# Optimization experiments

Measured on AMD Instinct MI355X. Metric: run time of the kernel, lower is better.

The kernel has to match this reference:

```python
import jax, jax.numpy as jnp
import numpy as np

D_MODEL = 2048
N_HEADS = 16
HEAD_DIM = D_MODEL // N_HEADS  # 128
B, S, PAST = 2, 2048, 2048


def setup_inputs() -> dict:
    key = jax.random.key(0)
    ks = jax.random.split(key, 7)
    sc = 0.02
    return {
        "x": jax.random.normal(ks[0], (B, S, D_MODEL), dtype=jnp.float32),
        "past_k": jax.random.normal(ks[1], (B, N_HEADS, PAST, HEAD_DIM), dtype=jnp.float32),
        "past_v": jax.random.normal(ks[2], (B, N_HEADS, PAST, HEAD_DIM), dtype=jnp.float32),
        "Wq": jax.random.normal(ks[3], (D_MODEL, D_MODEL), dtype=jnp.float32) * sc,
        "Wk": jax.random.normal(ks[4], (D_MODEL, D_MODEL), dtype=jnp.float32) * sc,
        "Wv": jax.random.normal(ks[5], (D_MODEL, D_MODEL), dtype=jnp.float32) * sc,
        "Wo": jax.random.normal(ks[6], (D_MODEL, D_MODEL), dtype=jnp.float32) * sc,
    }


def reference(x, past_k, past_v, Wq, Wk, Wv, Wo):
    b, s, d = x.shape
    # nn.Linear(bias=False): y = x @ W.T ; split heads -> (B, H, S, hd)
    def proj_heads(W):
        return (x @ W.T).reshape(b, s, N_HEADS, HEAD_DIM).transpose(0, 2, 1, 3)
    q = proj_heads(Wq)
    k = proj_heads(Wk)
    v = proj_heads(Wv)
    # KV-cache append along sequence axis
    k = jnp.concatenate([past_k, k], axis=2)  # (B, H, full_S, hd)
    v = jnp.concatenate([past_v, v], axis=2)
    present = (k, v)
    full_s = k.shape[2]
    scores = jnp.einsum("bhqd,bhkd->bhqk", q, k) / (HEAD_DIM ** 0.5)
    # causal mask: query i (global pos past+i) may attend keys j <= past+i
    offset = full_s - s
    qi = jnp.arange(s)[:, None]
    kj = jnp.arange(full_s)[None, :]
    mask = kj > (qi + offset)  # triu with diagonal = full_s - s + 1
    scores = jnp.where(mask[None, None], -jnp.inf, scores)
    attn = jax.nn.softmax(scores, axis=-1)
    out = jnp.einsum("bhqk,bhkd->bhqd", attn, v)
    out = out.transpose(0, 2, 1, 3).reshape(b, s, d)
    output = out @ Wo.T
    return output, present
```

## Files before the change

### kernel.cpp

```cpp
#include <hip/hip_runtime.h>
#include <hip/hip_bf16.h>
#include <stdint.h>

typedef __attribute__((ext_vector_type(8))) short bf16x8;
typedef __attribute__((ext_vector_type(4))) float f32x4;
typedef __attribute__((ext_vector_type(16))) float f32x16;
typedef unsigned short u16;
typedef unsigned int u32;
typedef const __attribute__((address_space(1))) u32* gp_t;
typedef __attribute__((address_space(3))) u32* lp_t;

#define HD 128
#define NH 16
#define SEQ 2048
#define PASTN 2048
#define FULLS 4096
#define DM 2048

__device__ __forceinline__ u16 f2b(float f){
  union { float f; u32 u; } v; v.f = f;
  return (u16)((v.u + 0x7fffu + ((v.u >> 16) & 1u)) >> 16);
}
__device__ __forceinline__ float b2f(u16 b){
  union { u32 u; float f; } v; v.u = ((u32)b) << 16;
  return v.f;
}
__device__ __forceinline__ u32 cvtpk(float lo, float hi){
  u32 r; asm("v_cvt_pk_bf16_f32 %0, %1, %2" : "=v"(r) : "v"(lo), "v"(hi)); return r;
}
__device__ __forceinline__ f32x16 zero16(){ f32x16 z = {}; return z; }

__global__ void k_conv5(const float* __restrict__ sx,
                        const float* __restrict__ s1, const float* __restrict__ s2,
                        const float* __restrict__ s3, const float* __restrict__ s4,
                        u16* __restrict__ dx,
                        u16* __restrict__ d1, u16* __restrict__ d2,
                        u16* __restrict__ d3, u16* __restrict__ d4)
{
  const int total = 2097152 + 4 * 1048576;
  int i = blockIdx.x * blockDim.x + threadIdx.x;
  int stride = gridDim.x * blockDim.x;
  for (; i < total; i += stride){
    const float* s; u16* d; int off;
    if (i < 2097152){ s = sx; d = dx; off = i; }
    else {
      int t = i - 2097152;
      int seg = t >> 20; off = t & 1048575;
      s = (seg == 0) ? s1 : (seg == 1) ? s2 : (seg == 2) ? s3 : s4;
      d = (seg == 0) ? d1 : (seg == 1) ? d2 : (seg == 2) ? d3 : d4;
    }
    float4 v = ((const float4*)s)[off];
    ushort4 o = { f2b(v.x), f2b(v.y), f2b(v.z), f2b(v.w) };
    ((ushort4*)d)[off] = o;
  }
}

__global__ __launch_bounds__(512, 1)
void k_qkv_fused(const u16* __restrict__ A,
                 const u16* __restrict__ Bq, const u16* __restrict__ Bk,
                 const u16* __restrict__ Bv,
                 u16* __restrict__ qb, u16* __restrict__ kbb,
                 u16* __restrict__ vtb,
                 float* __restrict__ outk, float* __restrict__ outv,
                 const float* __restrict__ pk, const float* __restrict__ pv)
{
  __shared__ char LDS[131072];
  const int bx = blockIdx.x;
  const int tid = threadIdx.x;

  if (bx >= 384){
    if (bx < 448){
      for (int i = (bx - 384) * 512 + tid; i < 2097152; i += 32768){
        int g = i * 4;
        int c = g & 127;
        int r = g >> 7;
        int bh = r >> 11;
        int s = r & 2047;
        long dst = ((long)bh * FULLS + s) * HD + c;
        float4 v = ((const float4*)pk)[i];
        *(float4*)(outk + dst) = v;
        ushort4 o = { f2b(v.x), f2b(v.y), f2b(v.z), f2b(v.w) };
        *(ushort4*)(kbb + dst) = o;
      }
    } else {
      float* ldsF = (float*)LDS;
      for (int cc = 0; cc < 16; cc++){
        int c = ((bx - 448) << 4) + cc;
        int bh = c >> 5, s0 = (c & 31) << 6;
        const float* src = pv + ((long)bh * PASTN + s0) * HD;
        float* dsv = outv + ((long)bh * FULLS + s0) * HD;
#pragma unroll
        for (int p = 0; p < 4; p++){
          int idx = tid + p * 512;
          int row = idx >> 5, c4 = (idx & 31) << 2;
          float4 v = *(const float4*)(src + row * HD + c4);
          *(float4*)(dsv + row * HD + c4) = v;
          ldsF[row * 129 + c4 + 0] = v.x;
          ldsF[row * 129 + c4 + 1] = v.y;
          ldsF[row * 129 + c4 + 2] = v.z;
          ldsF[row * 129 + c4 + 3] = v.w;
        }
        __syncthreads();
        int d = tid >> 2, sb = (tid & 3) << 4;
        u16* dst = vtb + ((long)bh * HD + d) * FULLS + s0 + sb;
#pragma unroll
        for (int g = 0; g < 4; g++){
          ushort4 o = { f2b(ldsF[(sb + g * 4 + 0) * 129 + d]),
                        f2b(ldsF[(sb + g * 4 + 1) * 129 + d]),
                        f2b(ldsF[(sb + g * 4 + 2) * 129 + d]),
                        f2b(ldsF[(sb + g * 4 + 3) * 129 + d]) };
          *(ushort4*)(dst + g * 4) = o;
        }
        __syncthreads();
      }
    }
    return;
  }

  const int w = tid >> 6, l = tid & 63;
  const int wm = w >> 2, wn = w & 3;
  const int which = bx >> 7;
  const int r0 = bx & 127;
  const int m0 = (r0 & 15) * 256;
  const int n0s = (r0 >> 4) * 256;
  const u16* Bm = (which == 0) ? Bq : (which == 1) ? Bk : Bv;

  const int aoff0 = (((l >> 4) * 16) ^ ((l & 7) << 4));
  const int aoff1 = ((64 + (l >> 4) * 16) ^ ((l & 7) << 4));
  const char* ArdB = LDS + wm * 16384 + (l & 15) * 128;
  const char* BrdB = LDS + 65536 + (wn >> 1) * 16384 + (wn & 1) * 8192 + (l & 15) * 128;

  const int Pa = tid * 16, Pb = tid * 16 + 8192;
  const int ra = Pa >> 7, rb = Pb >> 7;
  const int sro1 = ra * 2048 + ((((Pa & 127) ^ ((ra & 7) << 4))) >> 1);
  const int sro2 = rb * 2048 + ((((Pb & 127) ^ ((rb & 7) << 4))) >> 1);
  char* sd1 = LDS + w * 1024;
  char* sd2 = LDS + w * 1024 + 8192;

  f32x4 acc[8][4] = {};

#define GLDS(SRC, DST) __builtin_amdgcn_global_load_lds((gp_t)(const void*)(SRC), (lp_t)(void*)(DST), 16, 0, 0)
#define STG(MAT, ROWB, C, REG) { const u16* s_ = (MAT) + (long)(ROWB) * 2048 + (C) * 64; \
    GLDS(s_ + sro1, sd1 + (REG)); GLDS(s_ + sro2, sd2 + (REG)); }
#define RDB(DST, PAR) { _Pragma("unroll") for (int nf = 0; nf < 4; nf++){ \
      DST[nf*2]   = *(const bf16x8*)(BrdB + (PAR)*32768 + nf*2048 + aoff0); \
      DST[nf*2+1] = *(const bf16x8*)(BrdB + (PAR)*32768 + nf*2048 + aoff1); } }
#define RDA(PAR, MF) \
      a0 = *(const bf16x8*)(ArdB + (PAR)*32768 + (MF)*2048 + aoff0); \
      a1 = *(const bf16x8*)(ArdB + (PAR)*32768 + (MF)*2048 + aoff1); \
      a2 = *(const bf16x8*)(ArdB + (PAR)*32768 + (MF+1)*2048 + aoff0); \
      a3 = *(const bf16x8*)(ArdB + (PAR)*32768 + (MF+1)*2048 + aoff1);
#define BARW { __builtin_amdgcn_s_barrier(); \
      asm volatile("s_waitcnt lgkmcnt(0)" ::: "memory"); \
      __builtin_amdgcn_sched_barrier(0); }
#define MM(BF, MF) { __builtin_amdgcn_s_setprio(1); \
      _Pragma("unroll") for (int nf = 0; nf < 4; nf++){ \
        acc[MF][nf]   = __builtin_amdgcn_mfma_f32_16x16x32_bf16(a0, BF[nf*2],   acc[MF][nf],   0,0,0); \
        acc[MF][nf]   = __builtin_amdgcn_mfma_f32_16x16x32_bf16(a1, BF[nf*2+1], acc[MF][nf],   0,0,0); \
        acc[MF+1][nf] = __builtin_amdgcn_mfma_f32_16x16x32_bf16(a2, BF[nf*2],   acc[MF+1][nf], 0,0,0); \
        acc[MF+1][nf] = __builtin_amdgcn_mfma_f32_16x16x32_bf16(a3, BF[nf*2+1], acc[MF+1][nf], 0,0,0); } \
      __builtin_amdgcn_s_setprio(0); }

  STG(A,  m0,        0, 0);
  STG(A,  m0 + 128,  0, 16384);
  STG(Bm, n0s,       0, 65536);
  STG(Bm, n0s + 128, 0, 81920);
  STG(Bm, n0s,       1, 98304);
  STG(Bm, n0s + 128, 1, 114688);
  asm volatile("s_waitcnt vmcnt(4)" ::: "memory");
  __builtin_amdgcn_s_barrier();

  for (int i = 0; i < 16; ++i){
    const int c1 = 2 * i + 1;
    const int cn = 2 * i + 2;
    const bool nlast = (i < 15);
    bf16x8 b0[8], b1[8];
    bf16x8 a0, a1, a2, a3;

    RDB(b0, 0); RDA(0, 0);
    STG(A, m0, c1, 32768);
    BARW; MM(b0, 0);
    __builtin_amdgcn_s_barrier();

    RDA(0, 2);
    STG(A, m0 + 128, c1, 49152);
    BARW; MM(b0, 2);
    __builtin_amdgcn_s_barrier();

    RDA(0, 4);
    if (nlast) STG(Bm, n0s, cn, 65536);
    BARW; MM(b0, 4);
    __builtin_amdgcn_s_barrier();

    RDA(0, 6);
    if (nlast) STG(Bm, n0s + 128, cn, 81920);
    BARW; MM(b0, 6);
    if (nlast) { asm volatile("s_waitcnt vmcnt(4)" ::: "memory"); }
    else       { asm volatile("s_waitcnt vmcnt(0)" ::: "memory"); }
    __builtin_amdgcn_s_barrier();

    RDB(b1, 1); RDA(1, 0);
    if (nlast) STG(A, m0, cn, 0);
    BARW; MM(b1, 0);
    __builtin_amdgcn_s_barrier();

    RDA(1, 2);
    if (nlast) STG(A, m0 + 128, cn, 16384);
    BARW; MM(b1, 2);
    __builtin_amdgcn_s_barrier();

    RDA(1, 4);
    if (nlast) STG(Bm, n0s, cn + 1, 98304);
    BARW; MM(b1, 4);
    __builtin_amdgcn_s_barrier();

    RDA(1, 6);
    if (nlast) STG(Bm, n0s + 128, cn + 1, 114688);
    BARW; MM(b1, 6);
    if (nlast) { asm volatile("s_waitcnt vmcnt(4)" ::: "memory"); }
    __builtin_amdgcn_s_barrier();
  }

#undef MM
#undef BARW
#undef RDA
#undef RDB
#undef STG
#undef GLDS

  const int rbase = m0 + wm * 128 + ((l >> 4) << 2);
  const int cb2 = n0s + wn * 64 + (l & 15);
#pragma unroll
  for (int mf = 0; mf < 8; mf++){
#pragma unroll
    for (int nf = 0; nf < 4; nf++){
      const int nl = cb2 + nf * 16;
      const int h = nl >> 7, dd = nl & 127;
      if (which == 2){
        const int mm = rbase + mf * 16;
        const int b = mm >> 11, s = mm & 2047;
        const int bh = b * NH + h;
        ushort4 pkv = { f2b(acc[mf][nf][0]), f2b(acc[mf][nf][1]), f2b(acc[mf][nf][2]), f2b(acc[mf][nf][3]) };
        *(ushort4*)(vtb + ((long)bh * HD + dd) * FULLS + PASTN + s) = pkv;
#pragma unroll
        for (int r = 0; r < 4; r++){
          long idx = ((long)bh * FULLS + PASTN + s + r) * HD + dd;
          outv[idx] = acc[mf][nf][r];
        }
      } else if (which == 1){
#pragma unroll
        for (int r = 0; r < 4; r++){
          const int mm = rbase + mf * 16 + r;
          const int b = mm >> 11, s = mm & 2047;
          long idx = (((long)(b * NH + h)) * FULLS + PASTN + s) * HD + dd;
          float v = acc[mf][nf][r];
          kbb[idx] = f2b(v);
          outk[idx] = v;
        }
      } else {
#pragma unroll
        for (int r = 0; r < 4; r++){
          const int mm = rbase + mf * 16 + r;
          const int b = mm >> 11, s = mm & 2047;
          qb[(((long)(b * NH + h)) * SEQ + s) * HD + dd] = f2b(acc[mf][nf][r]);
        }
      }
    }
  }
}

__global__ void k_gemm_o(const u16* __restrict__ A, const u16* __restrict__ Bm,
                         float* __restrict__ outf, int M, int N, int K)
{
  __shared__ u16 As[128 * 64];
  __shared__ u16 Bs[128 * 64];
  const int tid = threadIdx.x;
  const int w = tid >> 6, l = tid & 63;
  const int m0 = blockIdx.y * 128, n0 = blockIdx.x * 128;
  const int wr = w >> 1, wc = w & 1;
  const int lr = l & 15;
  const int lkb = (l >> 4) * 16;
  f32x4 acc[4][4] = {};

  for (int kt = 0; kt < K; kt += 64){
#pragma unroll
    for (int it = 0; it < 4; it++){
      int Pw = it * 4096 + w * 1024;
      int P = Pw + l * 16;
      int row = P >> 7, cb = P & 127;
      const u16* ga = A + (long)(m0 + row) * K + kt + (cb >> 1);
      __builtin_amdgcn_global_load_lds((gp_t)(const void*)ga, (lp_t)(void*)((char*)As + Pw), 16, 0, 0);
      const u16* gb = Bm + (long)(n0 + row) * K + kt + (cb >> 1);
      __builtin_amdgcn_global_load_lds((gp_t)(const void*)gb, (lp_t)(void*)((char*)Bs + Pw), 16, 0, 0);
    }
    __syncthreads();
#pragma unroll
    for (int kk = 0; kk < 2; kk++){
      bf16x8 af[4], bf[4];
#pragma unroll
      for (int i = 0; i < 4; i++){
        af[i] = *(const bf16x8*)((const char*)As + (wr * 64 + i * 16 + lr) * 128 + kk * 64 + lkb);
        bf[i] = *(const bf16x8*)((const char*)Bs + (wc * 64 + i * 16 + lr) * 128 + kk * 64 + lkb);
      }
#pragma unroll
      for (int i = 0; i < 4; i++)
#pragma unroll
        for (int j = 0; j < 4; j++)
          acc[i][j] = __builtin_amdgcn_mfma_f32_16x16x32_bf16(af[i], bf[j], acc[i][j], 0, 0, 0);
    }
    __syncthreads();
  }

  const int rbase = m0 + wr * 64 + ((l >> 4) << 2);
  const int cbase = n0 + wc * 64 + lr;
#pragma unroll
  for (int i = 0; i < 4; i++)
#pragma unroll
    for (int j = 0; j < 4; j++){
      const int nn = cbase + j * 16;
#pragma unroll
      for (int r = 0; r < 4; r++)
        outf[(long)(rbase + i * 16 + r) * N + nn] = acc[i][j][r];
    }
}

__global__ __launch_bounds__(256, 2)
void k_attn(const u16* __restrict__ qb, const u16* __restrict__ kb,
            const u16* __restrict__ vtb, u16* __restrict__ ab)
{
  __shared__ u16 Ks[2][64 * 128];
  __shared__ u16 Vs[2][128 * 64];
  const int tid = threadIdx.x, w = tid >> 6, l = tid & 63;
  const int lq = l & 31, hi = l >> 5;
  const int dd0 = blockIdx.x;
  const int xcd = dd0 & 7;
  const int j   = dd0 >> 3;
  const int ja = j >> 5, jb = (j >> 1) & 15, jc = j & 1;
  const int bh  = xcd * 4 + 2 * ja + jc;
  const int q0b = ((ja ^ jc) ? (15 - jb) : jb) << 7;
  const int qbase = q0b + w * 32;
  const int qpos = PASTN + qbase + lq;
  const u16* qhead = qb + (long)bh * SEQ * HD;
  const u16* khead = kb + (long)bh * FULLS * HD;
  const u16* vhead = vtb + (long)bh * HD * FULLS;

  const float qscale = 0.08838834764831845f * 1.4426950408889634f;
  bf16x8 qf[8];
#pragma unroll
  for (int ks = 0; ks < 8; ks++){
    bf16x8 tq = *(const bf16x8*)(qhead + (long)(qbase + lq) * HD + ks * 16 + hi * 8);
#pragma unroll
    for (int jj = 0; jj < 8; jj++) tq[jj] = (short)f2b(b2f((u16)tq[jj]) * qscale);
    qf[ks] = tq;
  }

  const int kswz = (lq & 15) << 4;
  const int vswz = (lq & 7) << 4;
  const char* kaddr[8];
#pragma unroll
  for (int ks = 0; ks < 8; ks++)
    kaddr[ks] = (const char*)Ks + lq * 256 + ((ks * 32 + hi * 16) ^ kswz);
  const char* vaddr[4];
#pragma unroll
  for (int ks2 = 0; ks2 < 4; ks2++)
    vaddr[ks2] = (const char*)Vs + lq * 128 + ((ks2 * 32 + hi * 16) ^ vswz);

  int ksrcoff[4], vsrcoff[4];
#pragma unroll
  for (int it = 0; it < 4; it++){
    int P = it * 4096 + w * 1024 + l * 16;
    ksrcoff[it] = P ^ (((P >> 8) & 15) << 4);
    int row = P >> 7;
    int cb = (P & 127) ^ ((row & 7) << 4);
    vsrcoff[it] = row * 8192 + cb;
  }

  auto stageK = [&](int t, int bufo){
    const char* src = (const char*)khead + ((long)t << 14);
    char* dstb = (char*)Ks + bufo + w * 1024;
#pragma unroll
    for (int it = 0; it < 4; it++)
      __builtin_amdgcn_global_load_lds((gp_t)(const void*)(src + ksrcoff[it]),
                                       (lp_t)(void*)(dstb + it * 4096), 16, 0, 0);
  };
  auto stageV = [&](int t, int bufo){
    const char* src = (const char*)vhead + ((long)t << 7);
    char* dstb = (char*)Vs + bufo + w * 1024;
#pragma unroll
    for (int it = 0; it < 4; it++)
      __builtin_amdgcn_global_load_lds((gp_t)(const void*)(src + vsrcoff[it]),
                                       (lp_t)(void*)(dstb + it * 4096), 16, 0, 0);
  };

  f32x16 acc[4] = {};
  float m_run = -1e30f, l_run = 0.f;
  const int ntiles = (PASTN + q0b + 128) >> 6;

  auto finishPV = [&](f32x16& sp0, f32x16& sp1, int vbufo){
    float a0[8];
#pragma unroll
    for (int i = 0; i < 8; i++)
      a0[i] = fmaxf(fmaxf(sp0[i], sp0[i + 8]), fmaxf(sp1[i], sp1[i + 8]));
    float mx = fmaxf(fmaxf(fmaxf(a0[0], a0[1]), fmaxf(a0[2], a0[3])),
                     fmaxf(fmaxf(a0[4], a0[5]), fmaxf(a0[6], a0[7])));
    { float xa = mx, xb = mx;
      asm("v_permlane32_swap_b32 %0, %1" : "+v"(xa), "+v"(xb));
      mx = fmaxf(xa, xb); }

    if (!__all(mx <= m_run + 8.f)){
      float mnew = fmaxf(m_run, mx);
      float corr = __builtin_exp2f(m_run - mnew);
      m_run = mnew; l_run *= corr;
#pragma unroll
      for (int r = 0; r < 16; r++){
        int qlr = (r & 3) + 8 * (r >> 2) + 4 * hi;
        float cr = __shfl(corr, qlr);
#pragma unroll
        for (int d2 = 0; d2 < 4; d2++) acc[d2][r] *= cr;
      }
    }

    float rs = 0.f;
#pragma unroll
    for (int r = 0; r < 16; r++){
      sp0[r] = __builtin_exp2f(sp0[r] - m_run); rs += sp0[r];
      sp1[r] = __builtin_exp2f(sp1[r] - m_run); rs += sp1[r];
    }
    { float ra = rs, rb = rs;
      asm("v_permlane32_swap_b32 %0, %1" : "+v"(ra), "+v"(rb));
      l_run += ra + rb; }

    bf16x8 pfrag[4];
#pragma unroll
    for (int kb2 = 0; kb2 < 2; kb2++){
      const f32x16& sp = kb2 ? sp1 : sp0;
#pragma unroll
      for (int half = 0; half < 2; half++){
        const int h8 = half * 8;
        u32 A0 = cvtpk(sp[h8 + 0], sp[h8 + 1]);
        u32 A1 = cvtpk(sp[h8 + 2], sp[h8 + 3]);
        u32 B0 = cvtpk(sp[h8 + 4], sp[h8 + 5]);
        u32 B1 = cvtpk(sp[h8 + 6], sp[h8 + 7]);
        asm("v_permlane32_swap_b32 %0, %1" : "+v"(A0), "+v"(B0));
        asm("v_permlane32_swap_b32 %0, %1" : "+v"(A1), "+v"(B1));
        union { u32 wd[4]; bf16x8 v; } F;
        F.wd[0] = A0; F.wd[1] = A1; F.wd[2] = B0; F.wd[3] = B1;
        pfrag[kb2 * 2 + half] = F.v;
      }
    }

    __builtin_amdgcn_s_setprio(1);
#pragma unroll
    for (int ks2 = 0; ks2 < 4; ks2++)
#pragma unroll
      for (int d2 = 0; d2 < 4; d2++){
        bf16x8 vf = *(const bf16x8*)(vaddr[ks2] + vbufo + d2 * 4096);
        acc[d2] = __builtin_amdgcn_mfma_f32_32x32x16_bf16(pfrag[ks2], vf, acc[d2], 0, 0, 0);
      }
    __builtin_amdgcn_s_setprio(0);
  };

#define QKT_MASK(T_, BUFC_, SC0_, SC1_)                                        \
  {                                                                            \
    SC0_ = zero16(); SC1_ = zero16();                                          \
    __builtin_amdgcn_s_setprio(1);                                             \
    _Pragma("unroll")                                                          \
    for (int ks = 0; ks < 8; ks++){                                            \
      bf16x8 kf0 = *(const bf16x8*)(kaddr[ks] + (BUFC_));                      \
      bf16x8 kf1 = *(const bf16x8*)(kaddr[ks] + (BUFC_) + 8192);               \
      SC0_ = __builtin_amdgcn_mfma_f32_32x32x16_bf16(kf0, qf[ks], SC0_, 0,0,0);\
      SC1_ = __builtin_amdgcn_mfma_f32_32x32x16_bf16(kf1, qf[ks], SC1_, 0,0,0);\
    }                                                                          \
    __builtin_amdgcn_s_setprio(0);                                             \
    const int kvb_ = (T_) * 64;                                                \
    if (kvb_ + 63 > PASTN + qbase){                                            \
      _Pragma("unroll")                                                        \
      for (int r = 0; r < 16; r++){                                            \
        int key = kvb_ + (r & 3) + 8 * (r >> 2) + 4 * hi;                      \
        if (key > qpos) SC0_[r] = -1e30f;                                      \
        if (key + 32 > qpos) SC1_[r] = -1e30f;                                 \
      }                                                                        \
    }                                                                          \
  }

#define STEP(T_, BUFC_, SP0_, SP1_, SC0_, SC1_)                                \
  {                                                                            \
    if ((T_) + 1 < ntiles) stageK((T_) + 1, (BUFC_) ^ 16384);                  \
    QKT_MASK(T_, BUFC_, SC0_, SC1_);                                           \
    finishPV(SP0_, SP1_, (BUFC_) ^ 16384);                                     \
    __syncthreads();                                                           \
    if ((T_) + 1 < ntiles) stageV((T_) + 1, (BUFC_) ^ 16384);                  \
  }

  f32x16 PA0, PA1, PB0, PB1;

  stageK(0, 0); stageV(0, 0);
  __syncthreads();

  stageK(1, 16384);
  QKT_MASK(0, 0, PA0, PA1);
  __syncthreads();
  stageV(1, 16384);

  for (int t = 1; t + 2 < ntiles; t += 2){
    STEP(t,     16384, PA0, PA1, PB0, PB1);
    STEP(t + 1, 0,     PB0, PB1, PA0, PA1);
  }
  STEP(ntiles - 1, 16384, PA0, PA1, PB0, PB1);
  finishPV(PB0, PB1, 16384);

#undef STEP
#undef QKT_MASK

  float inv = 1.0f / l_run;
  const int b = bh >> 4, h = bh & 15;
#pragma unroll
  for (int r = 0; r < 16; r++){
    int qlr = (r & 3) + 8 * (r >> 2) + 4 * hi;
    float ir = __shfl(inv, qlr);
    long rowbase = ((long)b * SEQ + (qbase + qlr)) * DM + h * HD;
#pragma unroll
    for (int d2 = 0; d2 < 4; d2++)
      ab[rowbase + d2 * 32 + lq] = f2b(acc[d2][r] * ir);
  }
}

extern "C" void kernel_launch(void* const* d_in, const int* in_sizes, int n_in,
                              void* d_out, int out_size, void* d_ws, size_t ws_size,
                              hipStream_t stream) {
  const float* x      = (const float*)d_in[0];
  const float* past_k = (const float*)d_in[1];
  const float* past_v = (const float*)d_in[2];
  const float* Wq     = (const float*)d_in[3];
  const float* Wk     = (const float*)d_in[4];
  const float* Wv     = (const float*)d_in[5];
  const float* Wo     = (const float*)d_in[6];

  float* out  = (float*)d_out;
  float* outk = out + 8388608;
  float* outv = out + 25165824;

  char* ws = (char*)d_ws;
  u16* wqb = (u16*)ws;
  u16* wkb = (u16*)(ws + 8388608);
  u16* wvb = (u16*)(ws + 16777216);
  u16* wob = (u16*)(ws + 25165824);
  u16* xb  = (u16*)(ws + 33554432);
  u16* qb  = (u16*)(ws + 50331648);
  u16* kb  = (u16*)(ws + 67108864);
  u16* vtb = (u16*)(ws + 100663296);
  u16* ab  = xb;

  k_conv5<<<2048, 256, 0, stream>>>(x, Wq, Wk, Wv, Wo, xb, wqb, wkb, wvb, wob);

  k_qkv_fused<<<512, 512, 0, stream>>>(xb, wqb, wkb, wvb,
                                       qb, kb, vtb, outk, outv,
                                       past_k, past_v);

  k_attn<<<512, 256, 0, stream>>>(qb, kb, vtb, ab);

  k_gemm_o<<<dim3(16, 32), 256, 0, stream>>>(ab, wob, out, 4096, 2048, 2048);
}
```

Measured before the change: 370.0 us.

## Rewrite output projection GEMM as 8-wave pipelined kernel with swizzled LDS

```diff
diff --git a/kernel.cpp b/kernel.cpp
--- a/kernel.cpp
+++ b/kernel.cpp
@@ -269,58 +269,125 @@
   }
 }
 
-__global__ void k_gemm_o(const u16* __restrict__ A, const u16* __restrict__ Bm,
-                         float* __restrict__ outf, int M, int N, int K)
+__global__ __launch_bounds__(512, 1)
+void k_gemm_o8(const u16* __restrict__ A, const u16* __restrict__ Bm,
+               float* __restrict__ outf)
 {
-  __shared__ u16 As[128 * 64];
-  __shared__ u16 Bs[128 * 64];
-  const int tid = threadIdx.x;
-  const int w = tid >> 6, l = tid & 63;
-  const int m0 = blockIdx.y * 128, n0 = blockIdx.x * 128;
-  const int wr = w >> 1, wc = w & 1;
-  const int lr = l & 15;
-  const int lkb = (l >> 4) * 16;
-  f32x4 acc[4][4] = {};
-
-  for (int kt = 0; kt < K; kt += 64){
-#pragma unroll
-    for (int it = 0; it < 4; it++){
-      int Pw = it * 4096 + w * 1024;
-      int P = Pw + l * 16;
-      int row = P >> 7, cb = P & 127;
-      const u16* ga = A + (long)(m0 + row) * K + kt + (cb >> 1);
-      __builtin_amdgcn_global_load_lds((gp_t)(const void*)ga, (lp_t)(void*)((char*)As + Pw), 16, 0, 0);
-      const u16* gb = Bm + (long)(n0 + row) * K + kt + (cb >> 1);
-      __builtin_amdgcn_global_load_lds((gp_t)(const void*)gb, (lp_t)(void*)((char*)Bs + Pw), 16, 0, 0);
-    }
-    __syncthreads();
-#pragma unroll
-    for (int kk = 0; kk < 2; kk++){
-      bf16x8 af[4], bf[4];
-#pragma unroll
-      for (int i = 0; i < 4; i++){
-        af[i] = *(const bf16x8*)((const char*)As + (wr * 64 + i * 16 + lr) * 128 + kk * 64 + lkb);
-        bf[i] = *(const bf16x8*)((const char*)Bs + (wc * 64 + i * 16 + lr) * 128 + kk * 64 + lkb);
-      }
-#pragma unroll
-      for (int i = 0; i < 4; i++)
-#pragma unroll
-        for (int j = 0; j < 4; j++)
-          acc[i][j] = __builtin_amdgcn_mfma_f32_16x16x32_bf16(af[i], bf[j], acc[i][j], 0, 0, 0);
-    }
-    __syncthreads();
-  }
-
-  const int rbase = m0 + wr * 64 + ((l >> 4) << 2);
-  const int cbase = n0 + wc * 64 + lr;
-#pragma unroll
-  for (int i = 0; i < 4; i++)
-#pragma unroll
-    for (int j = 0; j < 4; j++){
-      const int nn = cbase + j * 16;
+  __shared__ char LDS[98304];
+  const int tid = threadIdx.x, w = tid >> 6, l = tid & 63;
+  const int wm = w >> 2, wn = w & 3;
+  const int m0 = (blockIdx.x & 15) * 256;
+  const int n0 = (blockIdx.x >> 4) * 128;
+
+  const int aoff0 = (((l >> 4) * 16) ^ ((l & 7) << 4));
+  const int aoff1 = ((64 + (l >> 4) * 16) ^ ((l & 7) << 4));
+  const char* ArdB = LDS + wm * 16384 + (l & 15) * 128;
+  const char* BrdB = LDS + 65536 + wn * 4096 + (l & 15) * 128;
+
+  const int Pa = tid * 16, Pb = tid * 16 + 8192;
+  const int ra = Pa >> 7, rb = Pb >> 7;
+  const int sro1 = ra * 2048 + ((((Pa & 127) ^ ((ra & 7) << 4))) >> 1);
+  const int sro2 = rb * 2048 + ((((Pb & 127) ^ ((rb & 7) << 4))) >> 1);
+  char* sd1 = LDS + w * 1024;
+  char* sd2 = LDS + w * 1024 + 8192;
+
+  f32x4 acc[8][2] = {};
+
+#define GLDS(SRC, DST) __builtin_amdgcn_global_load_lds((gp_t)(const void*)(SRC), (lp_t)(void*)(DST), 16, 0, 0)
+#define STG(MAT, ROWB, C, REG) { const u16* s_ = (MAT) + (long)(ROWB) * 2048 + (C) * 64; \
+    GLDS(s_ + sro1, sd1 + (REG)); GLDS(s_ + sro2, sd2 + (REG)); }
+#define RDB2(DST, PAR) { _Pragma("unroll") for (int nf = 0; nf < 2; nf++){ \
+      DST[nf*2]   = *(const bf16x8*)(BrdB + (PAR)*16384 + nf*2048 + aoff0); \
+      DST[nf*2+1] = *(const bf16x8*)(BrdB + (PAR)*16384 + nf*2048 + aoff1); } }
+#define RDA(PAR, MF) \
+      a0 = *(const bf16x8*)(ArdB + (PAR)*32768 + (MF)*2048 + aoff0); \
+      a1 = *(const bf16x8*)(ArdB + (PAR)*32768 + (MF)*2048 + aoff1); \
+      a2 = *(const bf16x8*)(ArdB + (PAR)*32768 + (MF+1)*2048 + aoff0); \
+      a3 = *(const bf16x8*)(ArdB + (PAR)*32768 + (MF+1)*2048 + aoff1);
+#define BARW { __builtin_amdgcn_s_barrier(); \
+      asm volatile("s_waitcnt lgkmcnt(0)" ::: "memory"); \
+      __builtin_amdgcn_sched_barrier(0); }
+#define MM2(BF, MF) { __builtin_amdgcn_s_setprio(1); \
+      _Pragma("unroll") for (int nf = 0; nf < 2; nf++){ \
+        acc[MF][nf]   = __builtin_amdgcn_mfma_f32_16x16x32_bf16(a0, BF[nf*2],   acc[MF][nf],   0,0,0); \
+        acc[MF][nf]   = __builtin_amdgcn_mfma_f32_16x16x32_bf16(a1, BF[nf*2+1], acc[MF][nf],   0,0,0); \
+        acc[MF+1][nf] = __builtin_amdgcn_mfma_f32_16x16x32_bf16(a2, BF[nf*2],   acc[MF+1][nf], 0,0,0); \
+        acc[MF+1][nf] = __builtin_amdgcn_mfma_f32_16x16x32_bf16(a3, BF[nf*2+1], acc[MF+1][nf], 0,0,0); } \
+      __builtin_amdgcn_s_setprio(0); }
+
+  STG(A,  m0,       0, 0);
+  STG(A,  m0 + 128, 0, 16384);
+  STG(Bm, n0,       0, 65536);
+  STG(Bm, n0,       1, 81920);
+  asm volatile("s_waitcnt vmcnt(2)" ::: "memory");
+  __builtin_amdgcn_s_barrier();
+
+  for (int i = 0; i < 16; ++i){
+    const int c1 = 2 * i + 1;
+    const int cn = 2 * i + 2;
+    const bool nlast = (i < 15);
+    bf16x8 b0[4], b1[4];
+    bf16x8 a0, a1, a2, a3;
+
+    RDB2(b0, 0); RDA(0, 0);
+    STG(A, m0, c1, 32768);
+    BARW; MM2(b0, 0);
+    __builtin_amdgcn_s_barrier();
+
+    RDA(0, 2);
+    STG(A, m0 + 128, c1, 49152);
+    BARW; MM2(b0, 2);
+    __builtin_amdgcn_s_barrier();
+
+    RDA(0, 4);
+    if (nlast) STG(Bm, n0, cn, 65536);
+    BARW; MM2(b0, 4);
+    __builtin_amdgcn_s_barrier();
+
+    RDA(0, 6);
+    BARW; MM2(b0, 6);
+    if (nlast) { asm volatile("s_waitcnt vmcnt(2)" ::: "memory"); }
+    else       { asm volatile("s_waitcnt vmcnt(0)" ::: "memory"); }
+    __builtin_amdgcn_s_barrier();
+
+    RDB2(b1, 1); RDA(1, 0);
+    if (nlast) STG(A, m0, cn, 0);
+    BARW; MM2(b1, 0);
+    __builtin_amdgcn_s_barrier();
+
+    RDA(1, 2);
+    if (nlast) STG(A, m0 + 128, cn, 16384);
+    BARW; MM2(b1, 2);
+    __builtin_amdgcn_s_barrier();
+
+    RDA(1, 4);
+    if (nlast) STG(Bm, n0, cn + 1, 81920);
+    BARW; MM2(b1, 4);
+    __builtin_amdgcn_s_barrier();
+
+    RDA(1, 6);
+    BARW; MM2(b1, 6);
+    if (nlast) { asm volatile("s_waitcnt vmcnt(2)" ::: "memory"); }
+    __builtin_amdgcn_s_barrier();
+  }
+
+#undef MM2
+#undef BARW
+#undef RDA
+#undef RDB2
+#undef STG
+#undef GLDS
+
+  const int rbase = m0 + wm * 128 + ((l >> 4) << 2);
+  const int cb2 = n0 + wn * 32 + (l & 15);
+#pragma unroll
+  for (int mf = 0; mf < 8; mf++)
+#pragma unroll
+    for (int nf = 0; nf < 2; nf++){
+      const int nn = cb2 + nf * 16;
 #pragma unroll
       for (int r = 0; r < 4; r++)
-        outf[(long)(rbase + i * 16 + r) * N + nn] = acc[i][j][r];
+        outf[(long)(rbase + mf * 16 + r) * DM + nn] = acc[mf][nf][r];
     }
 }
 
@@ -559,5 +626,5 @@
 
   k_attn<<<512, 256, 0, stream>>>(qb, kb, vtb, ab);
 
-  k_gemm_o<<<dim3(16, 32), 256, 0, stream>>>(ab, wob, out, 4096, 2048, 2048);
-}
+  k_gemm_o8<<<256, 512, 0, stream>>>(ab, wob, out);
+}
```

Result: faster. 355.7 us (median of 3 runs) (-3.9%).
